# Kernel tuning notes

Measured on AMD Instinct MI355X. Metric: run time of the kernel, lower is better.

Reference implementation:

```python
import jax, jax.numpy as jnp
import numpy as np


def _gelu(x):
    # torch nn.GELU default is the exact erf form
    return jax.nn.gelu(x, approximate=False)


def setup_inputs() -> dict:
    key = jax.random.key(0)
    B, C, H, W = 4, 64, 256, 256   # batch, width, grid
    L, M1, M2 = 2, 32, 32          # retained blocks, Fourier modes per corner
    HM, P, O = 128, 256, 1         # channel-MLP hidden, projection hidden, out channels
    ks = jax.random.split(key, 16)
    n = lambda k, s, sc=1.0: jax.random.normal(k, s, dtype=jnp.float32) * sc
    spec = 1.0 / (C * C)           # classic FNO spectral-weight init scale
    fan = 1.0 / np.sqrt(C).astype(np.float32)
    return {
        "x": n(ks[0], (B, C, H, W)),
        # spectral weights: last dim 2 = (real, imag); sw1 -> low-freq corner, sw2 -> high-freq corner
        "sw1": n(ks[1], (L, C, C, M1, M2, 2), spec),
        "sw2": n(ks[2], (L, C, C, M1, M2, 2), spec),
        "skip_w": n(ks[3], (L, C, C), fan),
        "skip_b": n(ks[4], (L, C), 0.01),
        "mlp_w1": n(ks[5], (L, HM, C), fan),
        "mlp_b1": n(ks[6], (L, HM), 0.01),
        "mlp_w2": n(ks[7], (L, C, HM), 1.0 / np.sqrt(HM).astype(np.float32)),
        "mlp_b2": n(ks[8], (L, C), 0.01),
        "mlp_skip_w": n(ks[9], (L, C, C), fan),
        "mlp_skip_b": n(ks[10], (L, C), 0.01),
        "proj_w1": n(ks[11], (P, C), fan),
        "proj_b1": n(ks[12], (P,), 0.01),
        "proj_w2": n(ks[13], (O, P), 1.0 / np.sqrt(P).astype(np.float32)),
        "proj_b2": n(ks[14], (O,), 0.01),
    }


def _chan(w, x, b):
    # 1x1 conv over channels: w [O,I], x [B,I,H,W], b [O]
    return jnp.einsum('oi,bihw->bohw', w, x) + b[None, :, None, None]


def reference(x, sw1, sw2, skip_w, skip_b, mlp_w1, mlp_b1, mlp_w2, mlp_b2,
              mlp_skip_w, mlp_skip_b, proj_w1, proj_b1, proj_w2, proj_b2):
    L, M1, M2 = sw1.shape[0], sw1.shape[3], sw1.shape[4]
    B, C, H, W = x.shape
    for l in range(L):
        # --- spectral convolution ---
        xft = jnp.fft.rfft2(x, axes=(-2, -1))            # [B,C,H,W//2+1] complex64
        w1 = sw1[l, ..., 0] + 1j * sw1[l, ..., 1]        # [C,C,M1,M2]
        w2 = sw2[l, ..., 0] + 1j * sw2[l, ..., 1]
        top = jnp.einsum('bixy,ioxy->boxy', xft[:, :, :M1, :M2], w1)
        bot = jnp.einsum('bixy,ioxy->boxy', xft[:, :, H - M1:, :M2], w2)
        oft = jnp.zeros(xft.shape, xft.dtype)
        oft = oft.at[:, :, :M1, :M2].set(top).at[:, :, H - M1:, :M2].set(bot)
        y = jnp.fft.irfft2(oft, s=(H, W), axes=(-2, -1))
        # --- pointwise skip + GELU ---
        x = _gelu(y + _chan(skip_w[l], x, skip_b[l]))
        # --- channel MLP (fc1 -> gelu -> fc2) with 1x1 skip + GELU ---
        h = _gelu(_chan(mlp_w1[l], x, mlp_b1[l]))
        y2 = _chan(mlp_w2[l], h, mlp_b2[l]) + _chan(mlp_skip_w[l], x, mlp_skip_b[l])
        x = _gelu(y2)
    # --- projection: fc1 -> gelu -> fc2 ---
    h = _gelu(_chan(proj_w1, x, proj_b1))
    return _chan(proj_w2, h, proj_b2)
```

## Files before the change

kernel.cpp:

```cpp
#include <hip/hip_runtime.h>
#include <math.h>


#define OFF_XA   0
#define OFF_XB   16777216
#define OFF_Z1   33554432
#define OFF_XF   37748736
#define OFF_OF   38797312
#define OFF_TBF  39845888
#define OFF_EH   39854080
#define OFF_EL   39862272
#define OFF_AFH  39870464
#define OFF_AFL  39903232
#define OFF_AIH  39936000
#define OFF_AIL  39968768
#define OFF_WBF  40001536


typedef __attribute__((ext_vector_type(8))) short short8b;
typedef __attribute__((ext_vector_type(4))) float f32x4;

__device__ __forceinline__ float gelu_f(float v) {
    float nu = v * fmaf(v * v, -0.10294345f, -2.3022078f);
    float e;
    asm("v_exp_f32 %0, %1" : "=v"(e) : "v"(nu));
    return v * __builtin_amdgcn_rcpf(1.0f + e);
}

__device__ __forceinline__ unsigned f2bf(float f) {
    unsigned int u = __float_as_uint(f);
    u += 0x7FFFu + ((u >> 16) & 1u);
    return u >> 16;
}

__device__ __forceinline__ unsigned cvtpk(float a, float b) {
    unsigned r;
    asm("v_cvt_pk_bf16_f32 %0, %1, %2" : "=v"(r) : "v"(a), "v"(b));
    return r;
}

__device__ __forceinline__ short8b ld_frag_i4(const unsigned short* base, int ch0, int px) {
    const uint2* p0 = (const uint2*)(base + (size_t)(ch0 >> 2) * 262144 + px * 4);
    const uint2* p1 = (const uint2*)(base + (size_t)((ch0 >> 2) + 1) * 262144 + px * 4);
    uint2 lo = *p0, hi = *p1;
    uint4 pk = {lo.x, lo.y, hi.x, hi.y};
    return *(short8b*)&pk;
}

__global__ __launch_bounds__(256) void init_tw(float* ws) {
    int idx = blockIdx.x * 256 + threadIdx.x;
    unsigned short* tbf = (unsigned short*)(ws + OFF_TBF);
    unsigned short* eh  = (unsigned short*)(ws + OFF_EH);
    unsigned short* el  = (unsigned short*)(ws + OFF_EL);
    unsigned short* afh = (unsigned short*)(ws + OFF_AFH);
    unsigned short* afl = (unsigned short*)(ws + OFF_AFL);
    unsigned short* aih = (unsigned short*)(ws + OFF_AIH);
    unsigned short* ail = (unsigned short*)(ws + OFF_AIL);
    const double PI128 = 3.14159265358979323846 / 128.0;
    if (idx < 16384) {
        int w = idx >> 6, k = idx & 63;
        int kx = k >> 1;
        int m = (kx * w) & 255;
        double a = (double)m * PI128;
        float sc = (kx == 0) ? (1.0f / 65536.0f) : (2.0f / 65536.0f);
        float v = (k & 1) ? (float)(-sin(a)) * sc : (float)cos(a) * sc;
        tbf[idx] = (unsigned short)f2bf(v);
    }
    int i2 = idx - 16384;
    if (i2 >= 0 && i2 < 16384) {
        int n = i2 >> 8, w = i2 & 255;
        int kx = n >> 1;
        int m = (kx * w) & 255;
        double a = (double)m * PI128;
        float v = (n & 1) ? (float)(-sin(a)) : (float)cos(a);
        unsigned h = f2bf(v);
        eh[i2] = (unsigned short)h;
        el[i2] = (unsigned short)f2bf(v - __uint_as_float(h << 16));
    }
    int i3 = idx - 32768;
    if (i3 >= 0 && i3 < 65536) {
        int n = i3 >> 9, k = i3 & 511;
        int j = n & 63, c = n >> 6;
        int h = k >> 1, d = k & 1;
        int ky = (j < 32) ? j : (192 + j);
        int m = (ky * h) & 255;
        double a = (double)m * PI128;
        float cv = (float)cos(a), sv = (float)sin(a);
        float v = (c == 0) ? (d ? sv : cv) : (d ? cv : -sv);
        unsigned hh = f2bf(v);
        afh[i3] = (unsigned short)hh;
        afl[i3] = (unsigned short)f2bf(v - __uint_as_float(hh << 16));
    }
    int i4 = idx - 98304;
    if (i4 >= 0 && i4 < 65536) {
        int c = i4 >> 15, rem = i4 & 32767;
        int h = rem >> 7, k = rem & 127;
        int j = k >> 1, d = k & 1;
        int ky = (j < 32) ? j : (192 + j);
        int m = (ky * h) & 255;
        double a = (double)m * PI128;
        float cv = (float)cos(a), sv = (float)sin(a);
        float v = (c == 0) ? (d ? -sv : cv) : (d ? cv : sv);
        unsigned hh = f2bf(v);
        aih[i4] = (unsigned short)hh;
        ail[i4] = (unsigned short)f2bf(v - __uint_as_float(hh << 16));
    }
}

__global__ __launch_bounds__(256) void k_cvt(const float* __restrict__ w1,
                                             const float* __restrict__ w2,
                                             const float* __restrict__ wsk,
                                             const float* __restrict__ pw1,
                                             const float* __restrict__ ssk,
                                             unsigned short* __restrict__ wb) {
    int idx = blockIdx.x * 256 + threadIdx.x;
    if (idx < 16384)       wb[idx] = (unsigned short)f2bf(w1[idx]);
    else if (idx < 32768)  wb[idx] = (unsigned short)f2bf(w2[idx - 16384]);
    else if (idx < 40960)  wb[idx] = (unsigned short)f2bf(wsk[idx - 32768]);
    else if (idx < 57344)  wb[idx] = (unsigned short)f2bf(pw1[idx - 40960]);
    else if (idx < 65536)  wb[idx] = (unsigned short)f2bf(ssk[idx - 57344]);
}

__global__ __launch_bounds__(256) void k_fwd_w_f32(const float* __restrict__ x,
                                                   float* __restrict__ X1f,
                                                   const unsigned short* __restrict__ EH,
                                                   const unsigned short* __restrict__ EL) {
    __shared__ __align__(16) unsigned short smEH[16384];
    __shared__ __align__(16) unsigned short smEL[16384];
    int t = threadIdx.x;
#pragma unroll
    for (int pass = 0; pass < 8; ++pass) {
        int g = pass * 256 + t;
        int rown = g >> 5, oct = g & 31;
        int dst = rown * 256 + ((oct ^ (rown & 7)) * 8);
        *(uint4*)&smEH[dst] = *(const uint4*)&EH[g * 8];
        *(uint4*)&smEL[dst] = *(const uint4*)&EL[g * 8];
    }
    __syncthreads();

    int lane = t & 63, wv = t >> 6;
    int col = lane & 15, grp = lane >> 4;
    size_t row0 = (size_t)blockIdx.x * 64;
    int row = wv * 16 + col;
    const float* rp = x + (row0 + row) * 256 + grp * 8;

    short8b bH[8], bL[8];
#pragma unroll
    for (int kb = 0; kb < 8; ++kb) {
        float4 v0 = *(const float4*)(rp + kb * 32);
        float4 v1 = *(const float4*)(rp + kb * 32 + 4);
        float vv[8] = {v0.x, v0.y, v0.z, v0.w, v1.x, v1.y, v1.z, v1.w};
        short8b vH, vL;
#pragma unroll
        for (int i = 0; i < 8; ++i) {
            unsigned h = f2bf(vv[i]);
            vH[i] = (short)h;
            vL[i] = (short)f2bf(vv[i] - __uint_as_float(h << 16));
        }
        bH[kb] = vH; bL[kb] = vL;
    }
#pragma unroll
    for (int ot = 0; ot < 4; ++ot) {
        int n = ot * 16 + col;
        const unsigned short* eh = &smEH[n * 256];
        const unsigned short* el = &smEL[n * 256];
        f32x4 acc = {0.f, 0.f, 0.f, 0.f};
#pragma unroll
        for (int kb = 0; kb < 8; ++kb) {
            int off = ((kb * 4 + grp) ^ (n & 7)) * 8;
            const short8b aH = *(const short8b*)&eh[off];
            const short8b aL = *(const short8b*)&el[off];
            acc = __builtin_amdgcn_mfma_f32_16x16x32_bf16(aH, bH[kb], acc, 0, 0, 0);
            acc = __builtin_amdgcn_mfma_f32_16x16x32_bf16(aH, bL[kb], acc, 0, 0, 0);
            acc = __builtin_amdgcn_mfma_f32_16x16x32_bf16(aL, bH[kb], acc, 0, 0, 0);
        }
        *(float4*)&X1f[(row0 + row) * 64 + ot * 16 + grp * 4] = *(float4*)&acc;
    }
}

__global__ __launch_bounds__(256) void k_fwd_w_bf16(const unsigned short* __restrict__ xb,
                                                    float* __restrict__ X1f,
                                                    const unsigned short* __restrict__ EH,
                                                    const unsigned short* __restrict__ EL) {
    __shared__ __align__(16) unsigned short smEH[16384];
    __shared__ __align__(16) unsigned short smEL[16384];
    int t = threadIdx.x;
#pragma unroll
    for (int pass = 0; pass < 8; ++pass) {
        int g = pass * 256 + t;
        int rown = g >> 5, oct = g & 31;
        int dst = rown * 256 + ((oct ^ (rown & 7)) * 8);
        *(uint4*)&smEH[dst] = *(const uint4*)&EH[g * 8];
        *(uint4*)&smEL[dst] = *(const uint4*)&EL[g * 8];
    }
    __syncthreads();

    int lane = t & 63, wv = t >> 6;
    int col = lane & 15, grp = lane >> 4;
    size_t row0 = (size_t)blockIdx.x * 64;
    int row = wv * 16 + col;
    const unsigned short* rp = xb + (row0 + row) * 256 + grp * 8;

    short8b bH[8];
#pragma unroll
    for (int kb = 0; kb < 8; ++kb)
        bH[kb] = *(const short8b*)(rp + kb * 32);
#pragma unroll
    for (int ot = 0; ot < 4; ++ot) {
        int n = ot * 16 + col;
        const unsigned short* eh = &smEH[n * 256];
        const unsigned short* el = &smEL[n * 256];
        f32x4 acc = {0.f, 0.f, 0.f, 0.f};
#pragma unroll
        for (int kb = 0; kb < 8; ++kb) {
            int off = ((kb * 4 + grp) ^ (n & 7)) * 8;
            const short8b aH = *(const short8b*)&eh[off];
            const short8b aL = *(const short8b*)&el[off];
            acc = __builtin_amdgcn_mfma_f32_16x16x32_bf16(aH, bH[kb], acc, 0, 0, 0);
            acc = __builtin_amdgcn_mfma_f32_16x16x32_bf16(aL, bH[kb], acc, 0, 0, 0);
        }
        *(float4*)&X1f[(row0 + row) * 64 + ot * 16 + grp * 4] = *(float4*)&acc;
    }
}

__global__ __launch_bounds__(256) void k_fwd_h(const float* __restrict__ X1f,
                                               float* __restrict__ XFre,
                                               float* __restrict__ XFim,
                                               const unsigned short* __restrict__ AFH,
                                               const unsigned short* __restrict__ AFL) {
    __shared__ __align__(16) unsigned short smH[32 * 512];
    int t = threadIdx.x;
    int plane = blockIdx.x;
    const float* xp = X1f + (size_t)plane * 16384;
#pragma unroll
    for (int pass = 0; pass < 16; ++pass) {
        int idx = pass * 256 + t;
        int h = idx >> 4, seg = idx & 15;
        float4 v = *(const float4*)(xp + h * 64 + seg * 4);
        int kx0 = seg * 2, kx1 = seg * 2 + 1;
        int k0 = 2 * h;
        int oct = k0 >> 3, e = k0 & 7;
        int b0 = oct ^ (kx0 & 7), b1 = oct ^ (kx1 & 7);
        *(unsigned*)&smH[kx0 * 512 + b0 * 8 + e] = cvtpk(v.x, v.y);
        *(unsigned*)&smH[kx1 * 512 + b1 * 8 + e] = cvtpk(v.z, v.w);
    }
    __syncthreads();
    int lane = t & 63, wv = t >> 6;
    int col = lane & 15, grp = lane >> 4;
#pragma unroll
    for (int mi = 0; mi < 2; ++mi) {
        int mt = wv * 2 + mi;
        const unsigned short* Ah = AFH + (mt * 16 + col) * 512;
        const unsigned short* Al = AFL + (mt * 16 + col) * 512;
        f32x4 acc0 = {0.f, 0.f, 0.f, 0.f}, acc1 = {0.f, 0.f, 0.f, 0.f};
#pragma unroll
        for (int kb = 0; kb < 16; ++kb) {
            short8b aH = *(const short8b*)&Ah[kb * 32 + grp * 8];
            short8b aL = *(const short8b*)&Al[kb * 32 + grp * 8];
#pragma unroll
            for (int nt = 0; nt < 2; ++nt) {
                int kx = nt * 16 + col;
                int blk = (kb * 4 + grp) ^ (kx & 7);
                short8b bH = *(const short8b*)&smH[kx * 512 + blk * 8];
                f32x4 a = (nt == 0) ? acc0 : acc1;
                a = __builtin_amdgcn_mfma_f32_16x16x32_bf16(aH, bH, a, 0, 0, 0);
                a = __builtin_amdgcn_mfma_f32_16x16x32_bf16(aL, bH, a, 0, 0, 0);
                if (nt == 0) acc0 = a; else acc1 = a;
            }
        }
#pragma unroll
        for (int nt = 0; nt < 2; ++nt) {
            int kx = nt * 16 + col;
            f32x4 a = (nt == 0) ? acc0 : acc1;
#pragma unroll
            for (int r = 0; r < 4; ++r) {
                int n = mt * 16 + grp * 4 + r;
                float* dst = (n < 64)
                    ? (XFre + (size_t)plane * 2048 + n * 32 + kx)
                    : (XFim + (size_t)plane * 2048 + (n - 64) * 32 + kx);
                *dst = a[r];
            }
        }
    }
}

__global__ __launch_bounds__(128) void k_modemul(const float* __restrict__ XFre,
                                                 const float* __restrict__ XFim,
                                                 const float2* __restrict__ sw1,
                                                 const float2* __restrict__ sw2,
                                                 float* __restrict__ OFT, int l) {
    int o0 = blockIdx.x * 4, j = blockIdx.y;
    int tid = threadIdx.x;
    int kx = tid & 31, b = tid >> 5;
    int jj = (j < 32) ? j : (j - 32);
    const float2* W0 = ((j < 32) ? sw1 : sw2)
                     + (l * 4194304 + (size_t)o0 * 1024 + jj * 32 + kx);
    const float* Xr = XFre + (size_t)(b * 64) * 2048 + j * 32 + kx;
    const float* Xi = XFim + (size_t)(b * 64) * 2048 + j * 32 + kx;
    float ar[4] = {0.f, 0.f, 0.f, 0.f}, ai[4] = {0.f, 0.f, 0.f, 0.f};
#pragma unroll 4
    for (int i = 0; i < 64; ++i) {
        float xr = Xr[i * 2048], xi = Xi[i * 2048];
        const float2* Wi = W0 + (size_t)i * 65536;
#pragma unroll
        for (int q = 0; q < 4; ++q) {
            float2 w = Wi[q * 1024];
            ar[q] += xr * w.x - xi * w.y;
            ai[q] += xr * w.y + xi * w.x;
        }
    }
#pragma unroll
    for (int q = 0; q < 4; ++q) {
        float* d = OFT + (size_t)(b * 64 + o0 + q) * 4096 + kx * 128 + 2 * j;
        d[0] = ar[q];
        d[1] = ai[q];
    }
}

__global__ __launch_bounds__(256) void k_inv_h(const float* __restrict__ OFT,
                                               float* __restrict__ Zre,
                                               float* __restrict__ Zim,
                                               const unsigned short* __restrict__ AIH,
                                               const unsigned short* __restrict__ AIL) {
    __shared__ __align__(16) unsigned short smH[32 * 128];
    int t = threadIdx.x;
    int plane = blockIdx.x;
    const float* op = OFT + (size_t)plane * 4096;
#pragma unroll
    for (int pass = 0; pass < 4; ++pass) {
        int idx = pass * 256 + t;
        int kx = idx >> 5, seg = idx & 31;
        float4 v = *(const float4*)(op + kx * 128 + seg * 4);
        int k0 = seg * 4;
        int oct = k0 >> 3, e = k0 & 7;
        int blk = oct ^ (kx & 7);
        uint2 ph = {cvtpk(v.x, v.y), cvtpk(v.z, v.w)};
        *(uint2*)&smH[kx * 128 + blk * 8 + e] = ph;
    }
    __syncthreads();
    int lane = t & 63, wv = t >> 6;
    int col = lane & 15, grp = lane >> 4;
#pragma unroll
    for (int mi = 0; mi < 4; ++mi) {
        int mt = wv * 4 + mi;
#pragma unroll
        for (int cc = 0; cc < 2; ++cc) {
            const unsigned short* Ah = AIH + cc * 32768 + (mt * 16 + col) * 128;
            const unsigned short* Al = AIL + cc * 32768 + (mt * 16 + col) * 128;
            f32x4 acc0 = {0.f, 0.f, 0.f, 0.f}, acc1 = {0.f, 0.f, 0.f, 0.f};
#pragma unroll
            for (int kb = 0; kb < 4; ++kb) {
                short8b aH = *(const short8b*)&Ah[kb * 32 + grp * 8];
                short8b aL = *(const short8b*)&Al[kb * 32 + grp * 8];
#pragma unroll
                for (int nt = 0; nt < 2; ++nt) {
                    int kx = nt * 16 + col;
                    int blk = (kb * 4 + grp) ^ (kx & 7);
                    short8b bH = *(const short8b*)&smH[kx * 128 + blk * 8];
                    f32x4 a = (nt == 0) ? acc0 : acc1;
                    a = __builtin_amdgcn_mfma_f32_16x16x32_bf16(aH, bH, a, 0, 0, 0);
                    a = __builtin_amdgcn_mfma_f32_16x16x32_bf16(aL, bH, a, 0, 0, 0);
                    if (nt == 0) acc0 = a; else acc1 = a;
                }
            }
            float* Zc = (cc == 0) ? Zre : Zim;
#pragma unroll
            for (int nt = 0; nt < 2; ++nt) {
                int kx = nt * 16 + col;
                f32x4 a = (nt == 0) ? acc0 : acc1;
#pragma unroll
                for (int r = 0; r < 4; ++r) {
                    int h = mt * 16 + grp * 4 + r;
                    Zc[(size_t)plane * 8192 + h * 32 + kx] = a[r];
                }
            }
        }
    }
}

template<int BF16IN>
__global__ __launch_bounds__(512) void k_invw_skip(const float* __restrict__ Zre,
                                                   const float* __restrict__ Zim,
                                                   const float* __restrict__ xinf,
                                                   const unsigned short* __restrict__ xinb,
                                                   const unsigned short* __restrict__ tbf,
                                                   const unsigned short* __restrict__ wsk,
                                                   const float* __restrict__ skip_b,
                                                   unsigned short* __restrict__ xout, int l) {
    __shared__ __align__(16) unsigned short smZ[64 * 64];
    int t = threadIdx.x;
    int hh = blockIdx.x, b = blockIdx.y;

    {
        int o = t >> 3, seg = t & 7;
        const float* zr = Zre + (size_t)(b * 64 + o) * 8192 + hh * 32 + seg * 4;
        const float* zi = Zim + (size_t)(b * 64 + o) * 8192 + hh * 32 + seg * 4;
        float4 r = *(const float4*)zr;
        float4 i = *(const float4*)zi;
        uint4 pk;
        pk.x = cvtpk(r.x, i.x);
        pk.y = cvtpk(r.y, i.y);
        pk.z = cvtpk(r.z, i.z);
        pk.w = cvtpk(r.w, i.w);
        int blk = seg ^ (o & 7);
        *(uint4*)&smZ[o * 64 + blk * 8] = pk;
    }

    int lane = t & 63, wv = t >> 6;
    int col = lane & 15, grp = lane >> 4;
    int w0 = wv * 32;

    short8b tf[2][2], bxf[2][2];
#pragma unroll
    for (int wt = 0; wt < 2; ++wt) {
        int w = w0 + wt * 16 + col;
#pragma unroll
        for (int kb = 0; kb < 2; ++kb) {
            tf[wt][kb] = *(const short8b*)&tbf[w * 64 + kb * 32 + grp * 8];
            int ch0 = kb * 32 + grp * 8;
            short8b v;
            if (BF16IN) {
                const unsigned short* xp = xinb + (size_t)(b * 64 + ch0) * 65536 + hh * 256 + w;
#pragma unroll
                for (int i = 0; i < 8; ++i) v[i] = (short)xp[(size_t)i * 65536];
            } else {
                const float* xp = xinf + (size_t)(b * 64 + ch0) * 65536 + hh * 256 + w;
#pragma unroll
                for (int i = 0; i < 8; ++i) v[i] = (short)f2bf(xp[(size_t)i * 65536]);
            }
            bxf[wt][kb] = v;
        }
    }
    __syncthreads();

    unsigned short* xo = xout + (size_t)b * 4194304;
    const unsigned short* WSp = wsk + l * 4096;
#pragma unroll
    for (int ot = 0; ot < 4; ++ot) {
        int o = ot * 16 + col;
        short8b az[2], ask[2];
#pragma unroll
        for (int kb = 0; kb < 2; ++kb) {
            int blk = (kb * 4 + grp) ^ (o & 7);
            az[kb] = *(const short8b*)&smZ[o * 64 + blk * 8];
            ask[kb] = *(const short8b*)&WSp[o * 64 + kb * 32 + grp * 8];
        }
        f32x4 bias = *(const f32x4*)&skip_b[l * 64 + ot * 16 + grp * 4];
#pragma unroll
        for (int wt = 0; wt < 2; ++wt) {
            f32x4 acc = bias;
            acc = __builtin_amdgcn_mfma_f32_16x16x32_bf16(az[0], tf[wt][0], acc, 0, 0, 0);
            acc = __builtin_amdgcn_mfma_f32_16x16x32_bf16(az[1], tf[wt][1], acc, 0, 0, 0);
            acc = __builtin_amdgcn_mfma_f32_16x16x32_bf16(ask[0], bxf[wt][0], acc, 0, 0, 0);
            acc = __builtin_amdgcn_mfma_f32_16x16x32_bf16(ask[1], bxf[wt][1], acc, 0, 0, 0);
            uint2 pk;
            pk.x = cvtpk(gelu_f(acc[0]), gelu_f(acc[1]));
            pk.y = cvtpk(gelu_f(acc[2]), gelu_f(acc[3]));
            int obase = ot * 16 + grp * 4;
            int px = hh * 256 + w0 + wt * 16 + col;
            *(uint2*)&xo[(size_t)(obase >> 2) * 262144 + px * 4] = pk;
        }
    }
}

template<int OUT4>
__global__ __launch_bounds__(512) void k_mlp(const unsigned short* __restrict__ xin,
                                             const unsigned short* __restrict__ wb,
                                             const float* __restrict__ b1,
                                             const float* __restrict__ b2,
                                             const float* __restrict__ bsk,
                                             unsigned short* __restrict__ xout, int l) {
    __shared__ __align__(16) unsigned short smemH[128 * 128];
    __shared__ __align__(16) unsigned short smW1[8192];
    __shared__ __align__(16) unsigned short smW2[8192];
    __shared__ __align__(16) unsigned short smWS[4096];
    int t = threadIdx.x;
    int b = blockIdx.y;
    int p0 = blockIdx.x * 128;

    const unsigned short* W1p = wb + l * 8192;
    const unsigned short* W2p = wb + 16384 + l * 8192;
    const unsigned short* WSp = wb + 32768 + l * 4096;
#pragma unroll
    for (int pass = 0; pass < 2; ++pass) {
        int g = pass * 512 + t;
        int row = g >> 3, oct = g & 7;
        *(uint4*)&smW1[row * 64 + ((oct ^ (row & 7)) * 8)] = *(const uint4*)&W1p[g * 8];
    }
#pragma unroll
    for (int pass = 0; pass < 2; ++pass) {
        int g = pass * 512 + t;
        int row = g >> 4, oct = g & 15;
        *(uint4*)&smW2[row * 128 + ((oct ^ (row & 7)) * 8)] = *(const uint4*)&W2p[g * 8];
    }
    if (t < 512) {
        int g = t;
        int row = g >> 3, oct = g & 7;
        *(uint4*)&smWS[row * 64 + ((oct ^ (row & 7)) * 8)] = *(const uint4*)&WSp[g * 8];
    }

    int lane = t & 63, wv = t >> 6;
    int col = lane & 15, grp = lane >> 4;
    int pxl = wv * 16 + col;
    int px = p0 + pxl;

    const unsigned short* xi = xin + (size_t)b * 4194304;
    short8b bx[2];
#pragma unroll
    for (int kb = 0; kb < 2; ++kb)
        bx[kb] = ld_frag_i4(xi, kb * 32 + grp * 8, px);
    __syncthreads();

#pragma unroll
    for (int ot = 0; ot < 8; ++ot) {
        int n1 = ot * 16 + col;
        short8b a0 = *(const short8b*)&smW1[n1 * 64 + ((grp ^ (n1 & 7)) * 8)];
        short8b a1 = *(const short8b*)&smW1[n1 * 64 + (((4 + grp) ^ (n1 & 7)) * 8)];
        int hm0 = ot * 16 + grp * 4;
        f32x4 acc = *(const f32x4*)&b1[l * 128 + hm0];
        acc = __builtin_amdgcn_mfma_f32_16x16x32_bf16(a0, bx[0], acc, 0, 0, 0);
        acc = __builtin_amdgcn_mfma_f32_16x16x32_bf16(a1, bx[1], acc, 0, 0, 0);
        uint2 hp;
        hp.x = cvtpk(gelu_f(acc[0]), gelu_f(acc[1]));
        hp.y = cvtpk(gelu_f(acc[2]), gelu_f(acc[3]));
        int blk = (hm0 >> 3) ^ (pxl & 7);
        *(uint2*)&smemH[pxl * 128 + blk * 8 + (hm0 & 7)] = hp;
    }

    short8b bh[4];
#pragma unroll
    for (int kb = 0; kb < 4; ++kb) {
        int blk = (kb * 4 + grp) ^ (pxl & 7);
        bh[kb] = *(const short8b*)&smemH[pxl * 128 + blk * 8];
    }

#pragma unroll
    for (int ot = 0; ot < 4; ++ot) {
        int o0 = ot * 16 + grp * 4;
        int n2 = ot * 16 + col;
        f32x4 acc = *(const f32x4*)&b2[l * 64 + o0];
        acc += *(const f32x4*)&bsk[l * 64 + o0];
        short8b a2[4], as[2];
#pragma unroll
        for (int kb = 0; kb < 4; ++kb)
            a2[kb] = *(const short8b*)&smW2[n2 * 128 + (((kb * 4 + grp) ^ (n2 & 7)) * 8)];
#pragma unroll
        for (int kb = 0; kb < 2; ++kb)
            as[kb] = *(const short8b*)&smWS[n2 * 64 + (((kb * 4 + grp) ^ (n2 & 7)) * 8)];
#pragma unroll
        for (int kb = 0; kb < 4; ++kb)
            acc = __builtin_amdgcn_mfma_f32_16x16x32_bf16(a2[kb], bh[kb], acc, 0, 0, 0);
#pragma unroll
        for (int kb = 0; kb < 2; ++kb)
            acc = __builtin_amdgcn_mfma_f32_16x16x32_bf16(as[kb], bx[kb], acc, 0, 0, 0);
        uint2 pk;
        pk.x = cvtpk(gelu_f(acc[0]), gelu_f(acc[1]));
        pk.y = cvtpk(gelu_f(acc[2]), gelu_f(acc[3]));
        if (OUT4) {
            unsigned short* xo = xout + (size_t)b * 4194304;
            *(uint2*)&xo[(size_t)(o0 >> 2) * 262144 + px * 4] = pk;
        } else {
            unsigned short* op = xout + (size_t)(b * 64 + o0) * 65536 + px;
            op[0]         = (unsigned short)(pk.x & 0xFFFF);
            op[65536]     = (unsigned short)(pk.x >> 16);
            op[2 * 65536] = (unsigned short)(pk.y & 0xFFFF);
            op[3 * 65536] = (unsigned short)(pk.y >> 16);
        }
    }
}

__global__ __launch_bounds__(512) void k_proj(const unsigned short* __restrict__ xin,
                                              const unsigned short* __restrict__ wb,
                                              const float* __restrict__ pb1,
                                              const float* __restrict__ pw2,
                                              const float* __restrict__ pb2,
                                              float* __restrict__ out) {
    __shared__ __align__(16) unsigned short smP1[16384];
    int t = threadIdx.x;
    int b = blockIdx.y;
    int p0 = blockIdx.x * 128;

    const unsigned short* P1p = wb + 40960;
#pragma unroll
    for (int pass = 0; pass < 4; ++pass) {
        int g = pass * 512 + t;
        int row = g >> 3, oct = g & 7;
        *(uint4*)&smP1[row * 64 + ((oct ^ (row & 7)) * 8)] = *(const uint4*)&P1p[g * 8];
    }

    int lane = t & 63, wv = t >> 6;
    int col = lane & 15, grp = lane >> 4;
    int px = p0 + wv * 16 + col;

    const unsigned short* xi = xin + (size_t)b * 4194304;
    short8b bx[2];
#pragma unroll
    for (int kb = 0; kb < 2; ++kb)
        bx[kb] = ld_frag_i4(xi, kb * 32 + grp * 8, px);
    __syncthreads();

    float psum = 0.f;
#pragma unroll
    for (int ot = 0; ot < 16; ++ot) {
        int n = ot * 16 + col;
        short8b a0 = *(const short8b*)&smP1[n * 64 + ((grp ^ (n & 7)) * 8)];
        short8b a1 = *(const short8b*)&smP1[n * 64 + (((4 + grp) ^ (n & 7)) * 8)];
        int o0 = ot * 16 + grp * 4;
        f32x4 b1v = *(const f32x4*)&pb1[o0];
        f32x4 w2v = *(const f32x4*)&pw2[o0];
        f32x4 acc = b1v;
        acc = __builtin_amdgcn_mfma_f32_16x16x32_bf16(a0, bx[0], acc, 0, 0, 0);
        acc = __builtin_amdgcn_mfma_f32_16x16x32_bf16(a1, bx[1], acc, 0, 0, 0);
        psum += w2v[0] * gelu_f(acc[0]) + w2v[1] * gelu_f(acc[1])
              + w2v[2] * gelu_f(acc[2]) + w2v[3] * gelu_f(acc[3]);
    }
    psum += __shfl_xor(psum, 16);
    psum += __shfl_xor(psum, 32);
    if (grp == 0)
        out[(size_t)b * 65536 + px] = psum + pb2[0];
}

extern "C" void kernel_launch(void* const* d_in, const int* in_sizes, int n_in,
                              void* d_out, int out_size, void* d_ws, size_t ws_size,
                              hipStream_t stream) {
    const float* x          = (const float*)d_in[0];
    const float2* sw1       = (const float2*)d_in[1];
    const float2* sw2       = (const float2*)d_in[2];
    const float* skip_w     = (const float*)d_in[3];
    const float* skip_b     = (const float*)d_in[4];
    const float* mlp_w1     = (const float*)d_in[5];
    const float* mlp_b1     = (const float*)d_in[6];
    const float* mlp_w2     = (const float*)d_in[7];
    const float* mlp_b2     = (const float*)d_in[8];
    const float* mlp_skip_w = (const float*)d_in[9];
    const float* mlp_skip_b = (const float*)d_in[10];
    const float* proj_w1    = (const float*)d_in[11];
    const float* proj_b1    = (const float*)d_in[12];
    const float* proj_w2    = (const float*)d_in[13];
    const float* proj_b2    = (const float*)d_in[14];

    float* ws = (float*)d_ws;
    unsigned short* XA4  = (unsigned short*)(ws + OFF_XA);
    unsigned short* XBb  = (unsigned short*)(ws + OFF_XB);
    unsigned short* XB4  = (unsigned short*)(ws + OFF_XB) + 16777216;
    float* X1f = ws + OFF_Z1;
    float* Zre = ws + OFF_Z1;
    float* Zim = ws + OFF_Z1 + 2097152;
    float* XFre = ws + OFF_XF;
    float* XFim = ws + OFF_XF + 524288;
    float* OFT = ws + OFF_OF;
    const unsigned short* TBF = (const unsigned short*)(ws + OFF_TBF);
    const unsigned short* EH  = (const unsigned short*)(ws + OFF_EH);
    const unsigned short* EL  = (const unsigned short*)(ws + OFF_EL);
    const unsigned short* AFH = (const unsigned short*)(ws + OFF_AFH);
    const unsigned short* AFL = (const unsigned short*)(ws + OFF_AFL);
    const unsigned short* AIH = (const unsigned short*)(ws + OFF_AIH);
    const unsigned short* AIL = (const unsigned short*)(ws + OFF_AIL);
    unsigned short* WB = (unsigned short*)(ws + OFF_WBF);

    init_tw<<<640, 256, 0, stream>>>(ws);
    k_cvt<<<256, 256, 0, stream>>>(mlp_w1, mlp_w2, mlp_skip_w, proj_w1, skip_w, WB);

    k_fwd_w_f32<<<1024, 256, 0, stream>>>(x, X1f, EH, EL);
    k_fwd_h<<<256, 256, 0, stream>>>(X1f, XFre, XFim, AFH, AFL);
    k_modemul<<<dim3(16, 64), 128, 0, stream>>>(XFre, XFim, sw1, sw2, OFT, 0);
    k_inv_h<<<256, 256, 0, stream>>>(OFT, Zre, Zim, AIH, AIL);
    k_invw_skip<0><<<dim3(256, 4), 512, 0, stream>>>(Zre, Zim, x, nullptr, TBF,
                                                     WB + 57344, skip_b, XA4, 0);
    k_mlp<0><<<dim3(512, 4), 512, 0, stream>>>(XA4, WB, mlp_b1, mlp_b2, mlp_skip_b, XBb, 0);

    k_fwd_w_bf16<<<1024, 256, 0, stream>>>(XBb, X1f, EH, EL);
    k_fwd_h<<<256, 256, 0, stream>>>(X1f, XFre, XFim, AFH, AFL);
    k_modemul<<<dim3(16, 64), 128, 0, stream>>>(XFre, XFim, sw1, sw2, OFT, 1);
    k_inv_h<<<256, 256, 0, stream>>>(OFT, Zre, Zim, AIH, AIL);
    k_invw_skip<1><<<dim3(256, 4), 512, 0, stream>>>(Zre, Zim, nullptr, XBb, TBF,
                                                     WB + 57344, skip_b, XA4, 1);
    k_mlp<1><<<dim3(512, 4), 512, 0, stream>>>(XA4, WB, mlp_b1, mlp_b2, mlp_skip_b, XB4, 1);

    k_proj<<<dim3(512, 4), 512, 0, stream>>>(XB4, WB, proj_b1, proj_w2, proj_b2,
                                             (float*)d_out);
}
```

Before: 296.1 us.

## Restructure spectral mode-multiply with LDS double-buffered async loads and split-K

Rewrites k_modemul so 512-thread blocks cover 32 output channels and stage spectral weights and Fourier inputs into LDS through double-buffered global_load_lds, with explicit vmcnt waits overlapping the next chunk's loads with the current chunk's complex FMAs. The input-channel reduction is split in two across blockIdx.z into two partial buffers, and k_inv_h sums them when it loads. The aim is better reuse of weights across batches, fewer redundant global loads and more memory parallelism in this bandwidth-bound step. The second partial buffer reuses the XA workspace region, which relies on XA being dead at that point in the schedule, and k_inv_h now reads twice as much.

```diff
diff --git a/kernel.cpp b/kernel.cpp
--- a/kernel.cpp
+++ b/kernel.cpp
@@ -37,6 +37,12 @@
     unsigned r;
     asm("v_cvt_pk_bf16_f32 %0, %1, %2" : "=v"(r) : "v"(a), "v"(b));
     return r;
+}
+
+__device__ __forceinline__ void gload_lds16(const void* g, void* l) {
+    __builtin_amdgcn_global_load_lds(
+        (const __attribute__((address_space(1))) unsigned int*)g,
+        (__attribute__((address_space(3))) unsigned int*)l, 16, 0, 0);
 }
 
 __device__ __forceinline__ short8b ld_frag_i4(const unsigned short* base, int ch0, int px) {
@@ -284,40 +290,99 @@
     }
 }
 
-__global__ __launch_bounds__(128) void k_modemul(const float* __restrict__ XFre,
+__global__ __launch_bounds__(512) void k_modemul(const float* __restrict__ XFre,
                                                  const float* __restrict__ XFim,
                                                  const float2* __restrict__ sw1,
                                                  const float2* __restrict__ sw2,
-                                                 float* __restrict__ OFT, int l) {
-    int o0 = blockIdx.x * 4, j = blockIdx.y;
-    int tid = threadIdx.x;
-    int kx = tid & 31, b = tid >> 5;
+                                                 float* __restrict__ OFT0,
+                                                 float* __restrict__ OFT1, int l) {
+    __shared__ __align__(16) unsigned char smBuf[2][36864];
+    int t = threadIdx.x;
+    int wv = t >> 6;
+    int o0 = blockIdx.x * 32;
+    int j  = blockIdx.y;
+    int ih = blockIdx.z;
     int jj = (j < 32) ? j : (j - 32);
-    const float2* W0 = ((j < 32) ? sw1 : sw2)
-                     + (l * 4194304 + (size_t)o0 * 1024 + jj * 32 + kx);
-    const float* Xr = XFre + (size_t)(b * 64) * 2048 + j * 32 + kx;
-    const float* Xi = XFim + (size_t)(b * 64) * 2048 + j * 32 + kx;
-    float ar[4] = {0.f, 0.f, 0.f, 0.f}, ai[4] = {0.f, 0.f, 0.f, 0.f};
-#pragma unroll 4
-    for (int i = 0; i < 64; ++i) {
-        float xr = Xr[i * 2048], xi = Xi[i * 2048];
-        const float2* Wi = W0 + (size_t)i * 65536;
-#pragma unroll
-        for (int q = 0; q < 4; ++q) {
-            float2 w = Wi[q * 1024];
-            ar[q] += xr * w.x - xi * w.y;
-            ai[q] += xr * w.y + xi * w.x;
-        }
-    }
-#pragma unroll
-    for (int q = 0; q < 4; ++q) {
-        float* d = OFT + (size_t)(b * 64 + o0 + q) * 4096 + kx * 128 + 2 * j;
-        d[0] = ar[q];
-        d[1] = ai[q];
-    }
+    const char* Wbase = (const char*)((j < 32) ? sw1 : sw2) + (size_t)l * 33554432
+                      + (size_t)jj * 256;
+    const char* XRb = (const char*)XFre + (size_t)j * 128;
+    const char* XIb = (const char*)XFim + (size_t)j * 128;
+    int ib0 = ih * 32;
+
+    auto STAGE = [&](int c, int buf) {
+        unsigned char* L = &smBuf[buf][0];
+#pragma unroll
+        for (int k = 0; k < 4; ++k) {
+            int g = k * 512 + t;
+            int gi = g >> 9, go = (g >> 4) & 31, gs = g & 15;
+            const char* src = Wbase + (size_t)(ib0 + c * 4 + gi) * 524288
+                            + (size_t)(o0 + go) * 8192 + gs * 16;
+            gload_lds16(src, L + g * 16);
+        }
+        if (t < 256) {
+            int d = t >> 7, b = (t >> 5) & 3, gi = (t >> 3) & 3, kq = t & 7;
+            const char* xb = d ? XIb : XRb;
+            const char* src = xb + (size_t)(b * 64 + ib0 + c * 4 + gi) * 8192 + kq * 16;
+            gload_lds16(src, L + 32768 + t * 16);
+        }
+    };
+
+    int oh = t >> 5, kx = t & 31;
+    float ar[2][4], ai[2][4];
+#pragma unroll
+    for (int oo = 0; oo < 2; ++oo)
+#pragma unroll
+        for (int b = 0; b < 4; ++b) { ar[oo][b] = 0.f; ai[oo][b] = 0.f; }
+
+    STAGE(0, 0);
+    for (int c = 0; c < 8; ++c) {
+        if (c + 1 < 8) {
+            STAGE(c + 1, (c + 1) & 1);
+            if (wv < 4) asm volatile("s_waitcnt vmcnt(5)" ::: "memory");
+            else        asm volatile("s_waitcnt vmcnt(4)" ::: "memory");
+        } else {
+            asm volatile("s_waitcnt vmcnt(0)" ::: "memory");
+        }
+        __builtin_amdgcn_sched_barrier(0);
+        __builtin_amdgcn_s_barrier();
+
+        const unsigned char* L = &smBuf[c & 1][0];
+#pragma unroll
+        for (int i = 0; i < 4; ++i) {
+            float2 w0 = *(const float2*)(L + (i * 32 + oh * 2) * 256 + kx * 8);
+            float2 w1 = *(const float2*)(L + (i * 32 + oh * 2 + 1) * 256 + kx * 8);
+            float xr[4], xi[4];
+#pragma unroll
+            for (int b = 0; b < 4; ++b) {
+                xr[b] = *(const float*)(L + 32768 + ((b * 4 + i) * 128) + kx * 4);
+                xi[b] = *(const float*)(L + 32768 + 2048 + ((b * 4 + i) * 128) + kx * 4);
+            }
+#pragma unroll
+            for (int b = 0; b < 4; ++b) {
+                ar[0][b] += xr[b] * w0.x - xi[b] * w0.y;
+                ai[0][b] += xr[b] * w0.y + xi[b] * w0.x;
+                ar[1][b] += xr[b] * w1.x - xi[b] * w1.y;
+                ai[1][b] += xr[b] * w1.y + xi[b] * w1.x;
+            }
+        }
+        asm volatile("s_waitcnt lgkmcnt(0)" ::: "memory");
+        __builtin_amdgcn_sched_barrier(0);
+        __builtin_amdgcn_s_barrier();
+    }
+
+    float* OP = (ih == 0) ? OFT0 : OFT1;
+#pragma unroll
+    for (int oo = 0; oo < 2; ++oo)
+#pragma unroll
+        for (int b = 0; b < 4; ++b) {
+            float* d = OP + (size_t)(b * 64 + o0 + oh * 2 + oo) * 4096 + kx * 128 + 2 * j;
+            d[0] = ar[oo][b];
+            d[1] = ai[oo][b];
+        }
 }
 
 __global__ __launch_bounds__(256) void k_inv_h(const float* __restrict__ OFT,
+                                               const float* __restrict__ OFT2,
                                                float* __restrict__ Zre,
                                                float* __restrict__ Zim,
                                                const unsigned short* __restrict__ AIH,
@@ -325,12 +390,15 @@
     __shared__ __align__(16) unsigned short smH[32 * 128];
     int t = threadIdx.x;
     int plane = blockIdx.x;
-    const float* op = OFT + (size_t)plane * 4096;
+    const float* op  = OFT  + (size_t)plane * 4096;
+    const float* op2 = OFT2 + (size_t)plane * 4096;
 #pragma unroll
     for (int pass = 0; pass < 4; ++pass) {
         int idx = pass * 256 + t;
         int kx = idx >> 5, seg = idx & 31;
-        float4 v = *(const float4*)(op + kx * 128 + seg * 4);
+        float4 v  = *(const float4*)(op  + kx * 128 + seg * 4);
+        float4 v2 = *(const float4*)(op2 + kx * 128 + seg * 4);
+        v.x += v2.x; v.y += v2.y; v.z += v2.z; v.w += v2.w;
         int k0 = seg * 4;
         int oct = k0 >> 3, e = k0 & 7;
         int blk = oct ^ (kx & 7);
@@ -649,6 +717,7 @@
     float* XFre = ws + OFF_XF;
     float* XFim = ws + OFF_XF + 524288;
     float* OFT = ws + OFF_OF;
+    float* OFT2 = ws + OFF_XA;
     const unsigned short* TBF = (const unsigned short*)(ws + OFF_TBF);
     const unsigned short* EH  = (const unsigned short*)(ws + OFF_EH);
     const unsigned short* EL  = (const unsigned short*)(ws + OFF_EL);
@@ -663,16 +732,16 @@
 
     k_fwd_w_f32<<<1024, 256, 0, stream>>>(x, X1f, EH, EL);
     k_fwd_h<<<256, 256, 0, stream>>>(X1f, XFre, XFim, AFH, AFL);
-    k_modemul<<<dim3(16, 64), 128, 0, stream>>>(XFre, XFim, sw1, sw2, OFT, 0);
-    k_inv_h<<<256, 256, 0, stream>>>(OFT, Zre, Zim, AIH, AIL);
+    k_modemul<<<dim3(2, 64, 2), 512, 0, stream>>>(XFre, XFim, sw1, sw2, OFT, OFT2, 0);
+    k_inv_h<<<256, 256, 0, stream>>>(OFT, OFT2, Zre, Zim, AIH, AIL);
     k_invw_skip<0><<<dim3(256, 4), 512, 0, stream>>>(Zre, Zim, x, nullptr, TBF,
                                                      WB + 57344, skip_b, XA4, 0);
     k_mlp<0><<<dim3(512, 4), 512, 0, stream>>>(XA4, WB, mlp_b1, mlp_b2, mlp_skip_b, XBb, 0);
 
     k_fwd_w_bf16<<<1024, 256, 0, stream>>>(XBb, X1f, EH, EL);
     k_fwd_h<<<256, 256, 0, stream>>>(X1f, XFre, XFim, AFH, AFL);
-    k_modemul<<<dim3(16, 64), 128, 0, stream>>>(XFre, XFim, sw1, sw2, OFT, 1);
-    k_inv_h<<<256, 256, 0, stream>>>(OFT, Zre, Zim, AIH, AIL);
+    k_modemul<<<dim3(2, 64, 2), 512, 0, stream>>>(XFre, XFim, sw1, sw2, OFT, OFT2, 1);
+    k_inv_h<<<256, 256, 0, stream>>>(OFT, OFT2, Zre, Zim, AIH, AIL);
     k_invw_skip<1><<<dim3(256, 4), 512, 0, stream>>>(Zre, Zim, nullptr, XBb, TBF,
                                                      WB + 57344, skip_b, XA4, 1);
     k_mlp<1><<<dim3(512, 4), 512, 0, stream>>>(XA4, WB, mlp_b1, mlp_b2, mlp_skip_b, XB4, 1);
```

New measurement: 286.3 us. -3.3%, faster.
